# Optimization experiments

Hardware: AMD Instinct MI355X
Metric: run time of the kernel (lower is better)

The kernel has to match this reference:

```python
import jax, jax.numpy as jnp
import numpy as np

N, E, G = 20000, 80000, 1000      # nodes, edges, graphs
F_TOT, EA = 16, 5                 # node feature dim, edge_attr dim
CSD = 5                           # cont_feat_start_dim
DIMS = [(5, 32), (32, 64), (64, 64)]  # NNConv (M_in, M_out) per layer
FC_IN = 64 + (F_TOT - CSD)        # 75


def setup_inputs() -> dict:
    key = jax.random.key(0)
    ks = iter(jax.random.split(key, 64))
    rnd = lambda sh: jax.random.normal(next(ks), sh, jnp.float32) * 0.1
    inp = {}
    inp["x"] = jax.random.normal(next(ks), (N, F_TOT), jnp.float32)
    inp["edge_index"] = jax.random.randint(next(ks), (2, E), 0, N)
    inp["edge_attr"] = jax.random.uniform(next(ks), (E, EA), dtype=jnp.float32)
    inp["batch"] = jnp.sort(jax.random.randint(next(ks), (N,), 0, G))
    for i, (mi, mo) in enumerate(DIMS, 1):
        inp[f"c{i}_w1"] = rnd((EA, 128))
        inp[f"c{i}_b1"] = jnp.zeros((128,), jnp.float32)
        inp[f"c{i}_w2"] = rnd((128, mi * mo))
        inp[f"c{i}_b2"] = jnp.zeros((mi * mo,), jnp.float32)
        inp[f"c{i}_root"] = rnd((mi, mo))
        inp[f"c{i}_bias"] = jnp.zeros((mo,), jnp.float32)
    inp["fc1_w"] = rnd((FC_IN, 32)); inp["fc1_b"] = jnp.zeros((32,), jnp.float32)
    inp["fc2_w"] = rnd((32, 16));    inp["fc2_b"] = jnp.zeros((16,), jnp.float32)
    inp["fc3_w"] = rnd((16, 1));     inp["fc3_b"] = jnp.zeros((1,), jnp.float32)
    return inp


def nnconv(h, edge_index, edge_attr, w1, b1, w2, b2, root, bias, mi, mo):
    # edge MLP -> per-edge [mi, mo] weight matrices
    hid = jax.nn.relu(edge_attr @ w1 + b1)                 # [E,128]
    W = (hid @ w2 + b2).reshape(-1, mi, mo)                # [E,mi,mo]
    src, dst = edge_index[0], edge_index[1]
    msg = jnp.einsum('ei,eio->eo', h[src], W)              # gather + per-edge matmul
    agg = jax.ops.segment_sum(msg, dst, num_segments=h.shape[0])  # scatter-add
    return agg + h @ root + bias


def reference(x, edge_index, edge_attr, batch,
              c1_w1, c1_b1, c1_w2, c1_b2, c1_root, c1_bias,
              c2_w1, c2_b1, c2_w2, c2_b2, c2_root, c2_bias,
              c3_w1, c3_b1, c3_w2, c3_b2, c3_root, c3_bias,
              fc1_w, fc1_b, fc2_w, fc2_b, fc3_w, fc3_b):
    convs = [(c1_w1, c1_b1, c1_w2, c1_b2, c1_root, c1_bias),
             (c2_w1, c2_b1, c2_w2, c2_b2, c2_root, c2_bias),
             (c3_w1, c3_b1, c3_w2, c3_b2, c3_root, c3_bias)]
    h = x[:, :CSD]
    for (w1, b1, w2, b2, root, bias), (mi, mo) in zip(convs, DIMS):
        h = jax.nn.elu(nnconv(h, edge_index, edge_attr, w1, b1, w2, b2, root, bias, mi, mo))
    x_int = h                                   # [N,64]
    x_cont = x[:, CSD:]                         # cont_feat_num_layers == 0
    hcat = jnp.concatenate([x_int, x_cont], axis=1)  # [N,75]
    # scatter_mean over graphs
    sums = jax.ops.segment_sum(hcat, batch, num_segments=G)
    cnts = jax.ops.segment_sum(jnp.ones((hcat.shape[0],), jnp.float32), batch, num_segments=G)
    g = sums / jnp.maximum(cnts, 1.0)[:, None]  # [G,75]
    g = jax.nn.elu(g @ fc1_w + fc1_b)
    g = jax.nn.elu(g @ fc2_w + fc2_b)
    g = g @ fc3_w + fc3_b
    return g.reshape(-1)
```

## Files before the change

kernel.cpp:

```cpp
#include <hip/hip_runtime.h>
#include <math.h>

constexpr int Nn = 20000;
constexpr int Ee = 80000;
constexpr int Gg = 1000;

typedef _Float16 f16x8 __attribute__((ext_vector_type(8)));
typedef _Float16 f16x4 __attribute__((ext_vector_type(4)));
typedef _Float16 f16x2 __attribute__((ext_vector_type(2)));
typedef float    f32x4 __attribute__((ext_vector_type(4)));

__device__ __forceinline__ float eluf(float x){ return x > 0.f ? x : (expf(x) - 1.f); }

__device__ __forceinline__ void bt_emit(int idx, int lgNF, int MIR, int s, int MO,
                                        const float* __restrict__ w2,
                                        const float* __restrict__ b2,
                                        _Float16* __restrict__ bt){
  int NF = 1 << lgNF;
  int j  = idx & 7;
  int l  = (idx >> 3) & 63;
  int n  = (idx >> 9) & (NF - 1);
  int ks = idx >> (9 + lgNF);
  int col = n * 16 + (l & 15);
  int kk  = ks * 32 + ((l >> 4) << 3) + j;
  int k = kk >> s, i = kk & ((1 << s) - 1);
  float v = 0.f;
  if (i < MIR){
    if (k < 128)       v = w2[(size_t)k * (MIR * MO) + i * MO + col];
    else if (k == 128) v = b2[i * MO + col];
  }
  bt[idx] = (_Float16)v;
}

__global__ void bt_all(const float* __restrict__ w21, const float* __restrict__ b21,
                       const float* __restrict__ w22, const float* __restrict__ b22,
                       const float* __restrict__ w23, const float* __restrict__ b23,
                       _Float16* __restrict__ bt1, _Float16* __restrict__ bt2,
                       _Float16* __restrict__ bt3){
  int idx = blockIdx.x * 256 + threadIdx.x;
  if (idx < 36864)                 bt_emit(idx,                1, 5,  3, 32, w21, b21, bt1);
  else if (idx < 36864 + 270336)   bt_emit(idx - 36864,        2, 32, 5, 64, w22, b22, bt2);
  else if (idx < 839680)           bt_emit(idx - 307200,       2, 64, 6, 64, w23, b23, bt3);
}

template<int MI, int MO>
__global__ void node_kernel(const float* __restrict__ h, int ldh,
                            const float* __restrict__ root,
                            const float* __restrict__ bias, float* __restrict__ agg){
  int idx = blockIdx.x * blockDim.x + threadIdx.x;
  if (idx >= Nn * MO) return;
  int n = idx / MO, o = idx - n * MO;
  float s = bias[o];
  #pragma unroll
  for (int i = 0; i < MI; ++i) s += h[(size_t)n * ldh + i] * root[i * MO + o];
  agg[idx] = s;
}

template<int MI, int MO>
__global__ __launch_bounds__(256) void elu_node_kernel(
    const float* __restrict__ agg_prev, const float* __restrict__ root,
    const float* __restrict__ bias, float* __restrict__ hout, float* __restrict__ agg_next){
  __shared__ float hl[32][MI + 1];
  int n0 = blockIdx.x * 32;
  int t  = threadIdx.x;
  for (int idx = t; idx < 32 * MI; idx += 256){
    int nl = idx / MI, i = idx - nl * MI;
    float v = eluf(agg_prev[(size_t)(n0 + nl) * MI + i]);
    hl[nl][i] = v;
    hout[(size_t)(n0 + nl) * MI + i] = v;
  }
  __syncthreads();
  for (int idx = t; idx < 32 * MO; idx += 256){
    int nl = idx / MO, o = idx - nl * MO;
    float s = bias[o];
    #pragma unroll 8
    for (int i = 0; i < MI; ++i) s += hl[nl][i] * root[i * MO + o];
    agg_next[(size_t)(n0 + nl) * MO + o] = s;
  }
}

template<int MIR, int MIP, int MO, int HIDK>
__global__ __launch_bounds__(256, 3) void edge_mfma(
    const float* __restrict__ ea, const float* __restrict__ w1, const float* __restrict__ b1,
    const _Float16* __restrict__ bt, const float* __restrict__ h, int ldh,
    const int* __restrict__ src, const int* __restrict__ dst, float* __restrict__ agg)
{
  constexpr int NF   = MO / 16;
  constexpr int NBLK = MIP / 8;
  constexpr int KS   = (HIDK * MIP) / 32;
  constexpr int HIDP = HIDK;
  constexpr int HID_B  = 64 * HIDP * 2;
  constexpr int HS_B   = 64 * MIP * 2;
  constexpr int COMB_B = 4 * 3 * NF * 64 * 16;
  constexpr int EA_O   = HID_B + HS_B;
  constexpr int SRC_O  = EA_O + 1280;
  constexpr int STG_E  = SRC_O + 256;
  constexpr int DST_O  = (STG_E > COMB_B) ? STG_E : COMB_B;

  __shared__ __align__(16) char pool[DST_O + 256];
  _Float16* hidp = (_Float16*)pool;
  _Float16* hsp  = (_Float16*)(pool + HID_B);
  float*    eap  = (float*)(pool + EA_O);
  int*      src_l = (int*)(pool + SRC_O);
  int*      dst_l = (int*)(pool + DST_O);

  const int tid  = threadIdx.x;
  const int lane = tid & 63;
  const int wave = tid >> 6;
  const int c15  = lane & 15;
  const int g    = lane >> 4;
  const int e0   = blockIdx.x * 64;

  const int ksb = ((KS * wave / 4) + 1) & ~1;
  const int kse = ((KS * (wave + 1) / 4) + 1) & ~1;
  const int KSW = kse - ksb;

  for (int t = tid; t < 320; t += 256) eap[t] = ea[(size_t)e0 * 5 + t];
  if (tid < 64){ src_l[tid] = src[e0 + tid]; dst_l[tid] = dst[e0 + tid]; }
  __syncthreads();

  for (int t = tid; t < 64 * HIDK; t += 256){
    int e = t / HIDK, k = t - e * HIDK;
    float s;
    if (k < 128){
      s = b1[k];
      #pragma unroll
      for (int j = 0; j < 5; ++j) s += eap[e * 5 + j] * w1[j * 128 + k];
      s = fmaxf(s, 0.f);
    } else s = (k == 128) ? 1.f : 0.f;
    hidp[e * HIDP + k] = (_Float16)s;
  }
  constexpr int IV = MIP / 4;
  for (int t = tid; t < 64 * IV; t += 256){
    int e = t / IV, i4 = (t - e * IV) * 4;
    f32x4 hv4 = *(const f32x4*)&h[(size_t)src_l[e] * ldh + i4];
    _Float16 o4[4];
    #pragma unroll
    for (int q = 0; q < 4; ++q) o4[q] = (i4 + q < MIR) ? (_Float16)hv4[q] : (_Float16)0.f;
    int bw = ((i4 >> 3) ^ (e & (NBLK - 1)));
    *(f16x4*)&hsp[e * MIP + ((bw << 3) | (i4 & 7))] = *(const f16x4*)o4;
  }
  __syncthreads();

  const f16x8* __restrict__ btv = (const f16x8*)bt;
  int er_[4];
  #pragma unroll
  for (int m = 0; m < 4; ++m) er_[m] = m * 16 + c15;

  f32x4 acc[4][NF];
  #pragma unroll
  for (int m = 0; m < 4; ++m)
    #pragma unroll
    for (int n = 0; n < NF; ++n) acc[m][n] = (f32x4){0.f, 0.f, 0.f, 0.f};

  f16x8 hsh[4][2];
  #pragma unroll
  for (int m = 0; m < 4; ++m){
    const int er = er_[m];
    if constexpr (MIP == 8){
      hsh[m][0] = *(const f16x8*)&hsp[er * MIP];
      hsh[m][1] = hsh[m][0];
    } else if constexpr (MIP == 32){
      int blk = g ^ (er & 3);
      hsh[m][0] = *(const f16x8*)&hsp[er * MIP + (blk << 3)];
      hsh[m][1] = hsh[m][0];
    } else {
      int b0 = g ^ (er & 7), b1x = (4 + g) ^ (er & 7);
      hsh[m][0] = *(const f16x8*)&hsp[er * MIP + (b0 << 3)];
      hsh[m][1] = *(const f16x8*)&hsp[er * MIP + (b1x << 3)];
    }
  }

  f16x8 bqA[NF], bqB[NF];
  #pragma unroll
  for (int n = 0; n < NF; ++n){
    bqA[n] = btv[((size_t)(ksb + 0) * NF + n) * 64 + lane];
    bqB[n] = btv[((size_t)(ksb + 1) * NF + n) * 64 + lane];
  }

#define EDGE_SUB(U, BQ)                                                         \
  {                                                                             \
    _Pragma("unroll")                                                           \
    for (int m = 0; m < 4; ++m){                                                \
      _Float16 hv;                                                              \
      f16x8 hs8;                                                                \
      if constexpr (MIP == 64){ hv = hvS[m]; hs8 = hsh[m][(U)]; }               \
      else if constexpr (MIP == 32){ hv = hv2[m][(U)]; hs8 = hsh[m][0]; }       \
      else { hv = hidp[er_[m] * HIDP + ((ksb + u + (U)) << 2) + g];             \
             hs8 = hsh[m][0]; }                                                 \
      f16x8 hvv = {hv, hv, hv, hv, hv, hv, hv, hv};                             \
      f16x8 av  = hs8 * hvv;                                                    \
      _Pragma("unroll")                                                         \
      for (int n = 0; n < NF; ++n)                                              \
        acc[m][n] = __builtin_amdgcn_mfma_f32_16x16x32_f16(av, BQ[n],           \
                                                           acc[m][n], 0, 0, 0);\
    }                                                                           \
    _Pragma("unroll")                                                           \
    for (int n = 0; n < NF; ++n)                                                \
      BQ[n] = btv[((size_t)(ksb + u + (U) + 2) * NF + n) * 64 + lane];          \
  }

  for (int u = 0; u < KSW; u += 2){
    _Float16 hvS[4]; f16x2 hv2[4];
    if constexpr (MIP == 64){
      #pragma unroll
      for (int m = 0; m < 4; ++m) hvS[m] = hidp[er_[m] * HIDP + ((ksb + u) >> 1)];
    } else if constexpr (MIP == 32){
      #pragma unroll
      for (int m = 0; m < 4; ++m) hv2[m] = *(const f16x2*)&hidp[er_[m] * HIDP + (ksb + u)];
    }
    (void)hvS; (void)hv2;
    EDGE_SUB(0, bqA)
    EDGE_SUB(1, bqB)
  }
#undef EDGE_SUB

  __syncthreads();
  float* comb = (float*)pool;
  #pragma unroll
  for (int m = 0; m < 4; ++m){
    if (m != wave){
      int s = wave - (wave > m ? 1 : 0);
      #pragma unroll
      for (int n = 0; n < NF; ++n)
        *(f32x4*)&comb[(((m * 3 + s) * NF + n) * 64 + lane) * 4] = acc[m][n];
    }
  }
  __syncthreads();
  #pragma unroll
  for (int m = 0; m < 4; ++m){
    if (m == wave){
      #pragma unroll
      for (int n = 0; n < NF; ++n){
        #pragma unroll
        for (int s = 0; s < 3; ++s)
          acc[m][n] += *(const f32x4*)&comb[(((m * 3 + s) * NF + n) * 64 + lane) * 4];
        #pragma unroll
        for (int j = 0; j < 4; ++j){
          int er = m * 16 + (g << 2) + j;
          atomicAdd(&agg[(size_t)dst_l[er] * MO + n * 16 + c15], acc[m][n][j]);
        }
      }
    }
  }
}

__global__ void zero_kernel(float* __restrict__ p, int n){
  int i = blockIdx.x * blockDim.x + threadIdx.x;
  if (i < n) p[i] = 0.f;
}

__global__ void pool_kernel(const float* __restrict__ agg3, const float* __restrict__ x,
                            const int* __restrict__ batch,
                            float* __restrict__ sums, float* __restrict__ cnts){
  int idx = blockIdx.x * blockDim.x + threadIdx.x;
  if (idx >= Nn * 75) return;
  int n = idx / 75, f = idx - n * 75;
  float v = (f < 64) ? eluf(agg3[(size_t)n * 64 + f]) : x[(size_t)n * 16 + 5 + (f - 64)];
  int b = batch[n];
  atomicAdd(&sums[(size_t)b * 75 + f], v);
  if (f == 0) atomicAdd(&cnts[b], 1.f);
}

__global__ __launch_bounds__(64) void head_kernel(
    const float* __restrict__ sums, const float* __restrict__ cnts,
    const float* __restrict__ fc1w, const float* __restrict__ fc1b,
    const float* __restrict__ fc2w, const float* __restrict__ fc2b,
    const float* __restrict__ fc3w, const float* __restrict__ fc3b,
    float* __restrict__ out)
{
  __shared__ float m[64][77];
  __shared__ float a1[64][33];
  __shared__ float a2[64][17];
  int t = threadIdx.x;
  int g = blockIdx.x * 64 + t;
  bool ok = g < Gg;
  float c = ok ? fmaxf(cnts[g], 1.f) : 1.f;
  for (int f = 0; f < 75; ++f) m[t][f] = ok ? sums[(size_t)g * 75 + f] / c : 0.f;
  for (int j = 0; j < 32; ++j){
    float s = fc1b[j];
    for (int f = 0; f < 75; ++f) s += m[t][f] * fc1w[f * 32 + j];
    a1[t][j] = eluf(s);
  }
  for (int j = 0; j < 16; ++j){
    float s = fc2b[j];
    for (int i = 0; i < 32; ++i) s += a1[t][i] * fc2w[i * 16 + j];
    a2[t][j] = eluf(s);
  }
  float s = fc3b[0];
  for (int i = 0; i < 16; ++i) s += a2[t][i] * fc3w[i];
  if (ok) out[g] = s;
}

extern "C" void kernel_launch(void* const* d_in, const int* in_sizes, int n_in,
                              void* d_out, int out_size, void* d_ws, size_t ws_size,
                              hipStream_t stream)
{
  (void)in_sizes; (void)n_in; (void)out_size; (void)ws_size;
  const float* x     = (const float*)d_in[0];
  const int*   ei    = (const int*)d_in[1];
  const float* ea    = (const float*)d_in[2];
  const int*   batch = (const int*)d_in[3];
  const float* cw1[3]   = {(const float*)d_in[4],  (const float*)d_in[10], (const float*)d_in[16]};
  const float* cb1[3]   = {(const float*)d_in[5],  (const float*)d_in[11], (const float*)d_in[17]};
  const float* cw2[3]   = {(const float*)d_in[6],  (const float*)d_in[12], (const float*)d_in[18]};
  const float* cb2[3]   = {(const float*)d_in[7],  (const float*)d_in[13], (const float*)d_in[19]};
  const float* croot[3] = {(const float*)d_in[8],  (const float*)d_in[14], (const float*)d_in[20]};
  const float* cbias[3] = {(const float*)d_in[9],  (const float*)d_in[15], (const float*)d_in[21]};
  const float* fc1w = (const float*)d_in[22];
  const float* fc1b = (const float*)d_in[23];
  const float* fc2w = (const float*)d_in[24];
  const float* fc2b = (const float*)d_in[25];
  const float* fc3w = (const float*)d_in[26];
  const float* fc3b = (const float*)d_in[27];
  float* out = (float*)d_out;

  float* ws   = (float*)d_ws;
  float* h    = ws;
  float* aggA = h + (size_t)Nn * 64;
  float* aggB = aggA + (size_t)Nn * 64;
  float* sums = aggB + (size_t)Nn * 64;
  float* cnts = sums + (size_t)Gg * 75;
  _Float16* bt1 = (_Float16*)(cnts + Gg);
  _Float16* bt2 = bt1 + 40960;
  _Float16* bt3 = bt2 + 278528;

  const int* src = ei;
  const int* dst = ei + Ee;

  bt_all<<<3280, 256, 0, stream>>>(cw2[0], cb2[0], cw2[1], cb2[1], cw2[2], cb2[2], bt1, bt2, bt3);

  node_kernel<5, 32><<<(Nn * 32 + 255) / 256, 256, 0, stream>>>(x, 16, croot[0], cbias[0], aggA);
  edge_mfma<5, 8, 32, 144><<<Ee / 64, 256, 0, stream>>>(ea, cw1[0], cb1[0], bt1, x, 16, src, dst, aggA);

  elu_node_kernel<32, 64><<<(Nn + 31) / 32, 256, 0, stream>>>(aggA, croot[1], cbias[1], h, aggB);
  edge_mfma<32, 32, 64, 132><<<Ee / 64, 256, 0, stream>>>(ea, cw1[1], cb1[1], bt2, h, 32, src, dst, aggB);

  elu_node_kernel<64, 64><<<(Nn + 31) / 32, 256, 0, stream>>>(aggB, croot[2], cbias[2], h, aggA);
  edge_mfma<64, 64, 64, 130><<<Ee / 64, 256, 0, stream>>>(ea, cw1[2], cb1[2], bt3, h, 64, src, dst, aggA);

  zero_kernel<<<(Gg * 76 + 255) / 256, 256, 0, stream>>>(sums, Gg * 76);
  pool_kernel<<<(Nn * 75 + 255) / 256, 256, 0, stream>>>(aggA, x, batch, sums, cnts);
  head_kernel<<<(Gg + 63) / 64, 64, 0, stream>>>(sums, cnts, fc1w, fc1b, fc2w, fc2b, fc3w, fc3b, out);
}
```

Before: 265.6 us.

## Unroll edge MFMA loop by four, halve combine buffer, fuse pooling and head

```diff
diff --git a/kernel.cpp b/kernel.cpp
--- a/kernel.cpp
+++ b/kernel.cpp
@@ -79,8 +79,8 @@
   }
 }
 
-template<int MIR, int MIP, int MO, int HIDK>
-__global__ __launch_bounds__(256, 3) void edge_mfma(
+template<int MIR, int MIP, int MO, int HIDK, int LB>
+__global__ __launch_bounds__(256, LB) void edge_mfma(
     const float* __restrict__ ea, const float* __restrict__ w1, const float* __restrict__ b1,
     const _Float16* __restrict__ bt, const float* __restrict__ h, int ldh,
     const int* __restrict__ src, const int* __restrict__ dst, float* __restrict__ agg)
@@ -88,10 +88,10 @@
   constexpr int NF   = MO / 16;
   constexpr int NBLK = MIP / 8;
   constexpr int KS   = (HIDK * MIP) / 32;
-  constexpr int HIDP = HIDK;
+  constexpr int HIDP = (MIP == 8) ? 148 : ((MIP == 32) ? 140 : 136);
   constexpr int HID_B  = 64 * HIDP * 2;
   constexpr int HS_B   = 64 * MIP * 2;
-  constexpr int COMB_B = 4 * 3 * NF * 64 * 16;
+  constexpr int COMB_B = 2 * 3 * NF * 64 * 16;
   constexpr int EA_O   = HID_B + HS_B;
   constexpr int SRC_O  = EA_O + 1280;
   constexpr int STG_E  = SRC_O + 256;
@@ -111,8 +111,8 @@
   const int g    = lane >> 4;
   const int e0   = blockIdx.x * 64;
 
-  const int ksb = ((KS * wave / 4) + 1) & ~1;
-  const int kse = ((KS * (wave + 1) / 4) + 1) & ~1;
+  const int ksb = ((KS * wave / 4) + 3) & ~3;
+  const int kse = (wave == 3) ? KS : ((KS * (wave + 1) / 4) + 3) & ~3;
   const int KSW = kse - ksb;
 
   for (int t = tid; t < 320; t += 256) eap[t] = ea[(size_t)e0 * 5 + t];
@@ -184,8 +184,8 @@
     for (int m = 0; m < 4; ++m){                                                \
       _Float16 hv;                                                              \
       f16x8 hs8;                                                                \
-      if constexpr (MIP == 64){ hv = hvS[m]; hs8 = hsh[m][(U)]; }               \
-      else if constexpr (MIP == 32){ hv = hv2[m][(U)]; hs8 = hsh[m][0]; }       \
+      if constexpr (MIP == 64){ hv = hvC2[m][(U) >> 1]; hs8 = hsh[m][(U) & 1]; }\
+      else if constexpr (MIP == 32){ hv = hvC4[m][(U)]; hs8 = hsh[m][0]; }      \
       else { hv = hidp[er_[m] * HIDP + ((ksb + u + (U)) << 2) + g];             \
              hs8 = hsh[m][0]; }                                                 \
       f16x8 hvv = {hv, hv, hv, hv, hv, hv, hv, hv};                             \
@@ -200,96 +200,135 @@
       BQ[n] = btv[((size_t)(ksb + u + (U) + 2) * NF + n) * 64 + lane];          \
   }
 
-  for (int u = 0; u < KSW; u += 2){
-    _Float16 hvS[4]; f16x2 hv2[4];
+  f16x2 hvC2[4], hvN2[4];
+  f16x4 hvC4[4], hvN4[4];
+  if constexpr (MIP == 64){
+    #pragma unroll
+    for (int m = 0; m < 4; ++m)
+      hvC2[m] = *(const f16x2*)&hidp[er_[m] * HIDP + (ksb >> 1)];
+  } else if constexpr (MIP == 32){
+    #pragma unroll
+    for (int m = 0; m < 4; ++m)
+      hvC4[m] = *(const f16x4*)&hidp[er_[m] * HIDP + ksb];
+  }
+
+  for (int u = 0; u < KSW; u += 4){
     if constexpr (MIP == 64){
       #pragma unroll
-      for (int m = 0; m < 4; ++m) hvS[m] = hidp[er_[m] * HIDP + ((ksb + u) >> 1)];
+      for (int m = 0; m < 4; ++m)
+        hvN2[m] = *(const f16x2*)&hidp[er_[m] * HIDP + ((ksb + u + 4) >> 1)];
     } else if constexpr (MIP == 32){
       #pragma unroll
-      for (int m = 0; m < 4; ++m) hv2[m] = *(const f16x2*)&hidp[er_[m] * HIDP + (ksb + u)];
+      for (int m = 0; m < 4; ++m)
+        hvN4[m] = *(const f16x4*)&hidp[er_[m] * HIDP + (ksb + u + 4)];
     }
-    (void)hvS; (void)hv2;
+    __builtin_amdgcn_s_setprio(1);
     EDGE_SUB(0, bqA)
     EDGE_SUB(1, bqB)
+    EDGE_SUB(2, bqA)
+    EDGE_SUB(3, bqB)
+    __builtin_amdgcn_s_setprio(0);
+    #pragma unroll
+    for (int m = 0; m < 4; ++m){ hvC2[m] = hvN2[m]; hvC4[m] = hvN4[m]; }
   }
 #undef EDGE_SUB
 
   __syncthreads();
   float* comb = (float*)pool;
   #pragma unroll
-  for (int m = 0; m < 4; ++m){
-    if (m != wave){
-      int s = wave - (wave > m ? 1 : 0);
-      #pragma unroll
-      for (int n = 0; n < NF; ++n)
-        *(f32x4*)&comb[(((m * 3 + s) * NF + n) * 64 + lane) * 4] = acc[m][n];
-    }
-  }
-  __syncthreads();
-  #pragma unroll
-  for (int m = 0; m < 4; ++m){
-    if (m == wave){
-      #pragma unroll
-      for (int n = 0; n < NF; ++n){
-        #pragma unroll
-        for (int s = 0; s < 3; ++s)
-          acc[m][n] += *(const f32x4*)&comb[(((m * 3 + s) * NF + n) * 64 + lane) * 4];
-        #pragma unroll
-        for (int j = 0; j < 4; ++j){
-          int er = m * 16 + (g << 2) + j;
-          atomicAdd(&agg[(size_t)dst_l[er] * MO + n * 16 + c15], acc[m][n][j]);
-        }
+  for (int m = 0; m < 2; ++m) if (m != wave){
+    int s = wave - (wave > m ? 1 : 0);
+    #pragma unroll
+    for (int n = 0; n < NF; ++n)
+      *(f32x4*)&comb[(((m * 3 + s) * NF + n) * 64 + lane) * 4] = acc[m][n];
+  }
+  __syncthreads();
+  #pragma unroll
+  for (int m = 0; m < 2; ++m) if (m == wave){
+    #pragma unroll
+    for (int n = 0; n < NF; ++n)
+      #pragma unroll
+      for (int s = 0; s < 3; ++s)
+        acc[m][n] += *(const f32x4*)&comb[(((m * 3 + s) * NF + n) * 64 + lane) * 4];
+  }
+  __syncthreads();
+  #pragma unroll
+  for (int m = 2; m < 4; ++m) if (m != wave){
+    int s = wave - (wave > m ? 1 : 0);
+    #pragma unroll
+    for (int n = 0; n < NF; ++n)
+      *(f32x4*)&comb[((((m - 2) * 3 + s) * NF + n) * 64 + lane) * 4] = acc[m][n];
+  }
+  __syncthreads();
+  #pragma unroll
+  for (int m = 2; m < 4; ++m) if (m == wave){
+    #pragma unroll
+    for (int n = 0; n < NF; ++n)
+      #pragma unroll
+      for (int s = 0; s < 3; ++s)
+        acc[m][n] += *(const f32x4*)&comb[((((m - 2) * 3 + s) * NF + n) * 64 + lane) * 4];
+  }
+  #pragma unroll
+  for (int m = 0; m < 4; ++m) if (m == wave){
+    #pragma unroll
+    for (int n = 0; n < NF; ++n)
+      #pragma unroll
+      for (int j = 0; j < 4; ++j){
+        int er = m * 16 + (g << 2) + j;
+        atomicAdd(&agg[(size_t)dst_l[er] * MO + n * 16 + c15], acc[m][n][j]);
       }
-    }
-  }
-}
-
-__global__ void zero_kernel(float* __restrict__ p, int n){
-  int i = blockIdx.x * blockDim.x + threadIdx.x;
-  if (i < n) p[i] = 0.f;
-}
-
-__global__ void pool_kernel(const float* __restrict__ agg3, const float* __restrict__ x,
-                            const int* __restrict__ batch,
-                            float* __restrict__ sums, float* __restrict__ cnts){
-  int idx = blockIdx.x * blockDim.x + threadIdx.x;
-  if (idx >= Nn * 75) return;
-  int n = idx / 75, f = idx - n * 75;
-  float v = (f < 64) ? eluf(agg3[(size_t)n * 64 + f]) : x[(size_t)n * 16 + 5 + (f - 64)];
-  int b = batch[n];
-  atomicAdd(&sums[(size_t)b * 75 + f], v);
-  if (f == 0) atomicAdd(&cnts[b], 1.f);
-}
-
-__global__ __launch_bounds__(64) void head_kernel(
-    const float* __restrict__ sums, const float* __restrict__ cnts,
+  }
+}
+
+__global__ __launch_bounds__(64) void pool_head_kernel(
+    const float* __restrict__ agg3, const float* __restrict__ x,
+    const int* __restrict__ batch,
     const float* __restrict__ fc1w, const float* __restrict__ fc1b,
     const float* __restrict__ fc2w, const float* __restrict__ fc2b,
     const float* __restrict__ fc3w, const float* __restrict__ fc3b,
     float* __restrict__ out)
 {
-  __shared__ float m[64][77];
-  __shared__ float a1[64][33];
-  __shared__ float a2[64][17];
-  int t = threadIdx.x;
-  int g = blockIdx.x * 64 + t;
-  bool ok = g < Gg;
-  float c = ok ? fmaxf(cnts[g], 1.f) : 1.f;
-  for (int f = 0; f < 75; ++f) m[t][f] = ok ? sums[(size_t)g * 75 + f] / c : 0.f;
-  for (int j = 0; j < 32; ++j){
-    float s = fc1b[j];
-    for (int f = 0; f < 75; ++f) s += m[t][f] * fc1w[f * 32 + j];
-    a1[t][j] = eluf(s);
-  }
-  for (int j = 0; j < 16; ++j){
-    float s = fc2b[j];
-    for (int i = 0; i < 32; ++i) s += a1[t][i] * fc2w[i * 16 + j];
-    a2[t][j] = eluf(s);
-  }
-  float s = fc3b[0];
-  for (int i = 0; i < 16; ++i) s += a2[t][i] * fc3w[i];
-  if (ok) out[g] = s;
+  int gph  = blockIdx.x;
+  int lane = threadIdx.x;
+  int lo = 0, hi = Nn;
+  while (lo < hi){ int mid = (lo + hi) >> 1; if (batch[mid] < gph) lo = mid + 1; else hi = mid; }
+  int start = lo;
+  hi = Nn;
+  while (lo < hi){ int mid = (lo + hi) >> 1; if (batch[mid] < gph + 1) lo = mid + 1; else hi = mid; }
+  int end = lo;
+
+  float s0 = 0.f, s1 = 0.f;
+  for (int n = start; n < end; ++n){
+    s0 += eluf(agg3[(size_t)n * 64 + lane]);
+    if (lane < 11) s1 += x[(size_t)n * 16 + 5 + lane];
+  }
+  float inv = 1.f / fmaxf((float)(end - start), 1.f);
+
+  __shared__ float m[75];
+  __shared__ float a1[32];
+  __shared__ float a2[16];
+  m[lane] = s0 * inv;
+  if (lane < 11) m[64 + lane] = s1 * inv;
+  __syncthreads();
+  if (lane < 32){
+    float s = fc1b[lane];
+    for (int f = 0; f < 75; ++f) s += m[f] * fc1w[f * 32 + lane];
+    a1[lane] = eluf(s);
+  }
+  __syncthreads();
+  if (lane < 16){
+    float s = fc2b[lane];
+    #pragma unroll
+    for (int i = 0; i < 32; ++i) s += a1[i] * fc2w[i * 16 + lane];
+    a2[lane] = eluf(s);
+  }
+  __syncthreads();
+  if (lane == 0){
+    float s = fc3b[0];
+    #pragma unroll
+    for (int i = 0; i < 16; ++i) s += a2[i] * fc3w[i];
+    out[gph] = s;
+  }
 }
 
 extern "C" void kernel_launch(void* const* d_in, const int* in_sizes, int n_in,
@@ -319,9 +358,7 @@
   float* h    = ws;
   float* aggA = h + (size_t)Nn * 64;
   float* aggB = aggA + (size_t)Nn * 64;
-  float* sums = aggB + (size_t)Nn * 64;
-  float* cnts = sums + (size_t)Gg * 75;
-  _Float16* bt1 = (_Float16*)(cnts + Gg);
+  _Float16* bt1 = (_Float16*)(aggB + (size_t)Nn * 64);
   _Float16* bt2 = bt1 + 40960;
   _Float16* bt3 = bt2 + 278528;
 
@@ -331,15 +368,13 @@
   bt_all<<<3280, 256, 0, stream>>>(cw2[0], cb2[0], cw2[1], cb2[1], cw2[2], cb2[2], bt1, bt2, bt3);
 
   node_kernel<5, 32><<<(Nn * 32 + 255) / 256, 256, 0, stream>>>(x, 16, croot[0], cbias[0], aggA);
-  edge_mfma<5, 8, 32, 144><<<Ee / 64, 256, 0, stream>>>(ea, cw1[0], cb1[0], bt1, x, 16, src, dst, aggA);
+  edge_mfma<5, 8, 32, 144, 4><<<Ee / 64, 256, 0, stream>>>(ea, cw1[0], cb1[0], bt1, x, 16, src, dst, aggA);
 
   elu_node_kernel<32, 64><<<(Nn + 31) / 32, 256, 0, stream>>>(aggA, croot[1], cbias[1], h, aggB);
-  edge_mfma<32, 32, 64, 132><<<Ee / 64, 256, 0, stream>>>(ea, cw1[1], cb1[1], bt2, h, 32, src, dst, aggB);
+  edge_mfma<32, 32, 64, 132, 3><<<Ee / 64, 256, 0, stream>>>(ea, cw1[1], cb1[1], bt2, h, 32, src, dst, aggB);
 
   elu_node_kernel<64, 64><<<(Nn + 31) / 32, 256, 0, stream>>>(aggB, croot[2], cbias[2], h, aggA);
-  edge_mfma<64, 64, 64, 130><<<Ee / 64, 256, 0, stream>>>(ea, cw1[2], cb1[2], bt3, h, 64, src, dst, aggA);
-
-  zero_kernel<<<(Gg * 76 + 255) / 256, 256, 0, stream>>>(sums, Gg * 76);
-  pool_kernel<<<(Nn * 75 + 255) / 256, 256, 0, stream>>>(aggA, x, batch, sums, cnts);
-  head_kernel<<<(Gg + 63) / 64, 64, 0, stream>>>(sums, cnts, fc1w, fc1b, fc2w, fc2b, fc3w, fc3b, out);
-}
+  edge_mfma<64, 64, 64, 130, 3><<<Ee / 64, 256, 0, stream>>>(ea, cw1[2], cb1[2], bt3, h, 64, src, dst, aggA);
+
+  pool_head_kernel<<<Gg, 64, 0, stream>>>(aggA, x, batch, fc1w, fc1b, fc2w, fc2b, fc3w, fc3b, out);
+}
```

New measurement: 221.9 us. -16.4%, faster.
